# Kernel tuning notes

Measured on AMD Instinct MI355X. Metric: run time of the kernel, lower is better.

## Reference

```python
import jax, jax.numpy as jnp
import numpy as np

H, W, C = 64, 64, 2048
IMG = 224


def setup_inputs() -> dict:
    key = jax.random.key(0)
    features = jax.random.normal(key, (2, H, W, C), dtype=jnp.float32)
    return {"features": features, "img_size": IMG}


def reference(features, img_size):
    # features: [2, H, W, C] -- query (index 0) and target (index 1) feature maps.
    x0 = features[0]  # [H, W, C]
    x1 = features[1]  # [H, W, C]
    # Correlation volume: Decomposition[i,j,k,l] = sum_c x0[i,j,c] * x1[k,l,c]
    # (replaces the quadruple Python loop with a single GEMM-shaped einsum)
    decom = jnp.einsum('ijc,klc->ijkl', x0, x1)  # [H, W, H, W]
    decom = decom / jnp.max(decom)
    # NOTE: source calls `Decomposition.clamp(min=0)` without assignment -> no-op.
    decom_1 = jnp.sum(decom, axis=(2, 3))  # [H, W] saliency on query image
    decom_2 = jnp.sum(decom, axis=(0, 1))  # [H, W] saliency on target image
    stacked = jnp.stack((decom_1, decom_2))  # [2, H, W]
    # F.interpolate(mode='bilinear', align_corners=False) == half-pixel bilinear resize
    out = jax.image.resize(stacked, (2, img_size, img_size), method='bilinear')
    return out  # [2, img_size, img_size]
```

## Files before the change

### kernel.cpp

```cpp
#include <hip/hip_runtime.h>
#include <hip/hip_bf16.h>

#define HW    4096
#define CDIM  2048
#define IMG   224
#define NTKI  64
#define NTM   128
#define LROW  528
#define QSCALE 21.166666f
#define NS    32
#define SBUF  24576

typedef int   int4v  __attribute__((ext_vector_type(4)));
typedef int   i32x16 __attribute__((ext_vector_type(16)));
typedef char  char4v __attribute__((ext_vector_type(4)));

__device__ __forceinline__ i32x16 zi16() {
    i32x16 z;
#pragma unroll
    for (int i = 0; i < 16; ++i) z[i] = 0;
    return z;
}
__device__ __forceinline__ char quant8(float x) {
    int r = __float2int_rn(x * QSCALE);
    r = min(max(r, -127), 127);
    return (char)r;
}

__device__ __forceinline__ void gload_lds16(const char* g, char* l) {
    __builtin_amdgcn_global_load_lds(
        (const __attribute__((address_space(1))) void*)g,
        (__attribute__((address_space(3))) void*)l, 16, 0, 0);
}

__global__ __launch_bounds__(256) void convert_pack_partial(
    const float* __restrict__ feat,
    char* __restrict__ Ap, char* __restrict__ Bp,
    float* __restrict__ P) {
    __shared__ char lds[64 * LROW];
    __shared__ float csum[512];
    const int tid = threadIdx.x;
    const int mat = blockIdx.z;
    const int rm  = blockIdx.y;
    const int kb0 = blockIdx.x * 512;
    const float* src = feat + (size_t)mat * HW * CDIM + (size_t)(rm * 64) * CDIM + kb0;

    const int cc = (tid & 127) * 4;
    float a0 = 0.f, a1 = 0.f, a2 = 0.f, a3 = 0.f;
#pragma unroll
    for (int j = 0; j < 32; ++j) {
        const int r = j * 2 + (tid >> 7);
        float4 v = *(const float4*)&src[(size_t)r * CDIM + cc];
        a0 += v.x; a1 += v.y; a2 += v.z; a3 += v.w;
        char4v q;
        q[0] = quant8(v.x); q[1] = quant8(v.y);
        q[2] = quant8(v.z); q[3] = quant8(v.w);
        *(char4v*)&lds[r * LROW + cc] = q;
    }
    if (tid >= 128) {
        csum[cc + 0] = a0; csum[cc + 1] = a1;
        csum[cc + 2] = a2; csum[cc + 3] = a3;
    }
    __syncthreads();
    if (tid < 128) {
        float4 p;
        p.x = a0 + csum[cc + 0]; p.y = a1 + csum[cc + 1];
        p.z = a2 + csum[cc + 2]; p.w = a3 + csum[cc + 3];
        *(float4*)&P[((size_t)mat * 64 + rm) * CDIM + kb0 + cc] = p;
    }

    const int l = tid & 63, w = tid >> 6;
    char* dstbase = mat ? Bp : Ap;
#pragma unroll
    for (int i = 0; i < 8; ++i) {
        const int t = w * 8 + i;
        const int tml = t >> 4, tkl = t & 15;
        int4v v = *(const int4v*)
            &lds[(tml * 32 + (l & 31)) * LROW + tkl * 32 + (l >> 5) * 16];
        const int tm  = rm * 2 + tml;
        const int tkg = blockIdx.x * 16 + tkl;
        *(int4v*)&dstbase[((size_t)(tm * NTKI + tkg) * 64 + l) * 16] = v;
    }
}

__global__ __launch_bounds__(512, 4) void gemm_max_kernel(
    const char* __restrict__ Ap, const char* __restrict__ Bp,
    const float* __restrict__ P, float* __restrict__ s,
    float* __restrict__ blockmax) {
    __shared__ char lds[3 * SBUF];
    __shared__ int wred[8];
    const int tid  = threadIdx.x;
    const int lane = tid & 63;
    const int wave = tid >> 6;
    const int wm = wave >> 1, wn = wave & 1;
    const int bm = blockIdx.y, bn = blockIdx.x;

    const char* gb[3];
    int loff[3];
#pragma unroll
    for (int q = 0; q < 3; ++q) {
        const int c = wave * 3 + q;
        const int kk = c & 1;
        if (c < 16) {
            const int il = c >> 1;
            gb[q] = Ap + ((size_t)(bm * 8 + il) * NTKI + kk) * 1024 + lane * 16;
            loff[q] = il * 2048 + kk * 1024;
        } else {
            const int jl = (c - 16) >> 1;
            gb[q] = Bp + ((size_t)(bn * 4 + jl) * NTKI + kk) * 1024 + lane * 16;
            loff[q] = 16384 + jl * 2048 + kk * 1024;
        }
    }

#define ISSUE_STAGE(S) do {                                         \
        char* buf_ = lds + ((S) % 3) * SBUF;                        \
        _Pragma("unroll")                                           \
        for (int q = 0; q < 3; ++q)                                 \
            gload_lds16(gb[q] + (size_t)(S) * 2048, buf_ + loff[q]);\
    } while (0)

    ISSUE_STAGE(0); ISSUE_STAGE(1);

    if (bm == 15 && bn < 16 && tid < 256) {
        const int gc = bn * 256 + tid;
        const float* Pp = P + (size_t)(gc >> 11) * 64 * CDIM + (gc & 2047);
        float sum = 0.f;
#pragma unroll 8
        for (int r = 0; r < 64; ++r) sum += Pp[(size_t)r * CDIM];
        s[gc] = sum;
    }

    asm volatile("s_waitcnt vmcnt(3)" ::: "memory");
    asm volatile("s_barrier" ::: "memory");

    const int aoff = wm * 2 * 2048 + lane * 16;
    const int boff = 16384 + wn * 2 * 2048 + lane * 16;

    i32x16 acc00 = zi16(), acc01 = zi16();
    i32x16 acc10 = zi16(), acc11 = zi16();

#define MM(i, j, A, B) acc##i##j = __builtin_amdgcn_mfma_i32_32x32x32_i8(A, B, acc##i##j, 0, 0, 0)

    for (int st = 0; st < NS; ++st) {
        const char* base = lds + (st % 3) * SBUF;
        const char* ab = base + aoff;
        const char* bb = base + boff;

        int4v a0k0 = *(const int4v*)(ab);
        int4v a1k0 = *(const int4v*)(ab + 2048);
        int4v a0k1 = *(const int4v*)(ab + 1024);
        int4v a1k1 = *(const int4v*)(ab + 2048 + 1024);
        int4v b0k0 = *(const int4v*)(bb);
        int4v b1k0 = *(const int4v*)(bb + 2048);
        int4v b0k1 = *(const int4v*)(bb + 1024);
        int4v b1k1 = *(const int4v*)(bb + 2048 + 1024);

        if (st + 2 < NS) ISSUE_STAGE(st + 2);

        __builtin_amdgcn_s_setprio(1);
        MM(0,0, a0k0, b0k0); MM(0,1, a0k0, b1k0);
        MM(1,0, a1k0, b0k0); MM(1,1, a1k0, b1k0);
        MM(0,0, a0k1, b0k1); MM(0,1, a0k1, b1k1);
        MM(1,0, a1k1, b0k1); MM(1,1, a1k1, b1k1);
        __builtin_amdgcn_s_setprio(0);

        if (st < NS - 2) { asm volatile("s_waitcnt vmcnt(3)" ::: "memory"); }
        else             { asm volatile("s_waitcnt vmcnt(0)" ::: "memory"); }
        if (st < NS - 1) { asm volatile("s_barrier" ::: "memory"); }
    }
#undef ISSUE_STAGE
#undef MM

    int m = INT_MIN;
#pragma unroll
    for (int i = 0; i < 16; ++i) {
        m = max(m, acc00[i]); m = max(m, acc01[i]);
        m = max(m, acc10[i]); m = max(m, acc11[i]);
    }
#pragma unroll
    for (int off = 32; off; off >>= 1)
        m = max(m, __shfl_down(m, off));
    if (lane == 0) wred[wave] = m;
    __syncthreads();
    if (tid == 0) {
        int im = wred[0];
#pragma unroll
        for (int w2 = 1; w2 < 8; ++w2) im = max(im, wred[w2]);
        blockmax[blockIdx.y * gridDim.x + blockIdx.x] =
            (float)im * (1.0f / (QSCALE * QSCALE));
    }
}

__global__ __launch_bounds__(256) void saliency_kernel(
    const float* __restrict__ feat, const float* __restrict__ s,
    float* __restrict__ sal) {
    const int tid = threadIdx.x, lane = tid & 63, wave = tid >> 6;
    const int g = blockIdx.x * 4 + wave;
    const float* x;
    const float* sv;
    if (g < HW) { x = feat + (size_t)g * CDIM;                            sv = s + CDIM; }
    else        { x = feat + (size_t)HW * CDIM + (size_t)(g - HW) * CDIM; sv = s; }
    float acc = 0.f;
#pragma unroll
    for (int it = 0; it < 8; ++it) {
        const int c0 = it * 256 + lane * 4;
        float4 v = *(const float4*)&x[c0];
        float4 w = *(const float4*)&sv[c0];
        acc += v.x * w.x + v.y * w.y + v.z * w.z + v.w * w.w;
    }
#pragma unroll
    for (int off = 32; off; off >>= 1) acc += __shfl_down(acc, off);
    if (lane == 0) sal[g] = acc;
}

__global__ __launch_bounds__(256) void resize_kernel(
    const float* __restrict__ sal, const float* __restrict__ bmax,
    float* __restrict__ out) {
    __shared__ float w[4];
    __shared__ float rM;
    const int tid = threadIdx.x;
    float m = -3.4e38f;
    for (int i = tid; i < 512; i += 256) m = fmaxf(m, bmax[i]);
#pragma unroll
    for (int off = 32; off; off >>= 1) m = fmaxf(m, __shfl_down(m, off));
    if ((tid & 63) == 0) w[tid >> 6] = m;
    __syncthreads();
    if (tid == 0)
        rM = 1.0f / fmaxf(fmaxf(w[0], w[1]), fmaxf(w[2], w[3]));
    __syncthreads();

    const int idx = blockIdx.x * 256 + tid;
    if (idx >= 2 * IMG * IMG) return;
    const int ch = idx / (IMG * IMG);
    const int rem = idx % (IMG * IMG);
    const int oy = rem / IMG, ox = rem % IMG;
    const float scale = 64.0f / (float)IMG;
    const float sy = ((float)oy + 0.5f) * scale - 0.5f;
    const float sx = ((float)ox + 0.5f) * scale - 0.5f;
    const float fy0 = floorf(sy), fx0 = floorf(sx);
    const float wy = sy - fy0, wx = sx - fx0;
    int y0 = (int)fy0, x0 = (int)fx0;
    int y1 = min(max(y0 + 1, 0), 63), x1 = min(max(x0 + 1, 0), 63);
    y0 = min(max(y0, 0), 63); x0 = min(max(x0, 0), 63);
    const float* p = sal + ch * HW;
    const float v00 = p[y0 * 64 + x0], v01 = p[y0 * 64 + x1];
    const float v10 = p[y1 * 64 + x0], v11 = p[y1 * 64 + x1];
    out[idx] = ((1.f - wy) * ((1.f - wx) * v00 + wx * v01) +
                wy * ((1.f - wx) * v10 + wx * v11)) * rM;
}

extern "C" void kernel_launch(void* const* d_in, const int* in_sizes, int n_in,
                              void* d_out, int out_size, void* d_ws, size_t ws_size,
                              hipStream_t stream) {
    const float* feat = (const float*)d_in[0];
    float* out = (float*)d_out;

    char* ws = (char*)d_ws;
    char* Ap = ws;
    char* Bp = ws + (size_t)8 * 1024 * 1024;
    float* P    = (float*)(ws + (size_t)16 * 1024 * 1024);
    float* s    = P + 2 * 64 * CDIM;
    float* bmax = s + 2 * CDIM;
    float* sal  = bmax + 1024;

    convert_pack_partial<<<dim3(4, 64, 2), 256, 0, stream>>>(feat, Ap, Bp, P);
    gemm_max_kernel<<<dim3(32, 16), 512, 0, stream>>>(Ap, Bp, P, s, bmax);
    saliency_kernel<<<2048, 256, 0, stream>>>(feat, s, sal);
    const int nout = 2 * IMG * IMG;
    resize_kernel<<<(nout + 255) / 256, 256, 0, stream>>>(sal, bmax, out);
}
```

Baseline: 140.5 us.

## Enlarge GEMM block tile to 256x256 with 4 waves and register double-buffering

The int8 correlation GEMM now uses 256 threads per block, each wave computing a 128x128 sub-tile (4x4 MFMA accumulators) over a 16x16 grid instead of 32x16. The triple-buffered LDS stage grows to 32 KB, and LDS fragment reads for the next stage are software-pipelined against MFMAs on the current stage using two register sets. The aim is more operand reuse per LDS byte and less global traffic per output. The cost is only 256 blocks, fewer than two per CU, with one block per CU allowed, plus heavy register and accumulator pressure.

```diff
diff --git a/kernel.cpp b/kernel.cpp
--- a/kernel.cpp
+++ b/kernel.cpp
@@ -9,7 +9,7 @@
 #define LROW  528
 #define QSCALE 21.166666f
 #define NS    32
-#define SBUF  24576
+#define SBUF3 32768
 
 typedef int   int4v  __attribute__((ext_vector_type(4)));
 typedef int   i32x16 __attribute__((ext_vector_type(16)));
@@ -83,23 +83,23 @@
     }
 }
 
-__global__ __launch_bounds__(512, 4) void gemm_max_kernel(
+__global__ __launch_bounds__(256, 1) void gemm_max_kernel(
     const char* __restrict__ Ap, const char* __restrict__ Bp,
     const float* __restrict__ P, float* __restrict__ s,
     float* __restrict__ blockmax) {
-    __shared__ char lds[3 * SBUF];
-    __shared__ int wred[8];
+    __shared__ char lds[3 * SBUF3];
+    __shared__ int wred[4];
     const int tid  = threadIdx.x;
     const int lane = tid & 63;
     const int wave = tid >> 6;
     const int wm = wave >> 1, wn = wave & 1;
     const int bm = blockIdx.y, bn = blockIdx.x;
 
-    const char* gb[3];
-    int loff[3];
-#pragma unroll
-    for (int q = 0; q < 3; ++q) {
-        const int c = wave * 3 + q;
+    const char* gb[8];
+    int loff[8];
+#pragma unroll
+    for (int q = 0; q < 8; ++q) {
+        const int c = wave * 8 + q;
         const int kk = c & 1;
         if (c < 16) {
             const int il = c >> 1;
@@ -107,21 +107,24 @@
             loff[q] = il * 2048 + kk * 1024;
         } else {
             const int jl = (c - 16) >> 1;
-            gb[q] = Bp + ((size_t)(bn * 4 + jl) * NTKI + kk) * 1024 + lane * 16;
+            gb[q] = Bp + ((size_t)(bn * 8 + jl) * NTKI + kk) * 1024 + lane * 16;
             loff[q] = 16384 + jl * 2048 + kk * 1024;
         }
     }
 
-#define ISSUE_STAGE(S) do {                                         \
-        char* buf_ = lds + ((S) % 3) * SBUF;                        \
+#define ISSUE_STAGE(S, BUF) do {                                    \
         _Pragma("unroll")                                           \
-        for (int q = 0; q < 3; ++q)                                 \
-            gload_lds16(gb[q] + (size_t)(S) * 2048, buf_ + loff[q]);\
+        for (int q = 0; q < 8; ++q)                                 \
+            gload_lds16(gb[q] + (size_t)(S) * 2048, (BUF) + loff[q]);\
     } while (0)
 
-    ISSUE_STAGE(0); ISSUE_STAGE(1);
-
-    if (bm == 15 && bn < 16 && tid < 256) {
+    char* r0 = lds;
+    char* r1 = lds + SBUF3;
+    char* r2 = lds + 2 * SBUF3;
+
+    ISSUE_STAGE(0, r0); ISSUE_STAGE(1, r1);
+
+    if (bm == 15 && bn < 16) {
         const int gc = bn * 256 + tid;
         const float* Pp = P + (size_t)(gc >> 11) * 64 * CDIM + (gc & 2047);
         float sum = 0.f;
@@ -130,62 +133,96 @@
         s[gc] = sum;
     }
 
-    asm volatile("s_waitcnt vmcnt(3)" ::: "memory");
+    asm volatile("s_waitcnt vmcnt(8)" ::: "memory");
     asm volatile("s_barrier" ::: "memory");
 
-    const int aoff = wm * 2 * 2048 + lane * 16;
-    const int boff = 16384 + wn * 2 * 2048 + lane * 16;
-
-    i32x16 acc00 = zi16(), acc01 = zi16();
-    i32x16 acc10 = zi16(), acc11 = zi16();
-
-#define MM(i, j, A, B) acc##i##j = __builtin_amdgcn_mfma_i32_32x32x32_i8(A, B, acc##i##j, 0, 0, 0)
-
-    for (int st = 0; st < NS; ++st) {
-        const char* base = lds + (st % 3) * SBUF;
-        const char* ab = base + aoff;
-        const char* bb = base + boff;
-
-        int4v a0k0 = *(const int4v*)(ab);
-        int4v a1k0 = *(const int4v*)(ab + 2048);
-        int4v a0k1 = *(const int4v*)(ab + 1024);
-        int4v a1k1 = *(const int4v*)(ab + 2048 + 1024);
-        int4v b0k0 = *(const int4v*)(bb);
-        int4v b1k0 = *(const int4v*)(bb + 2048);
-        int4v b0k1 = *(const int4v*)(bb + 1024);
-        int4v b1k1 = *(const int4v*)(bb + 2048 + 1024);
-
-        if (st + 2 < NS) ISSUE_STAGE(st + 2);
-
-        __builtin_amdgcn_s_setprio(1);
-        MM(0,0, a0k0, b0k0); MM(0,1, a0k0, b1k0);
-        MM(1,0, a1k0, b0k0); MM(1,1, a1k0, b1k0);
-        MM(0,0, a0k1, b0k1); MM(0,1, a0k1, b1k1);
-        MM(1,0, a1k1, b0k1); MM(1,1, a1k1, b1k1);
-        __builtin_amdgcn_s_setprio(0);
-
-        if (st < NS - 2) { asm volatile("s_waitcnt vmcnt(3)" ::: "memory"); }
-        else             { asm volatile("s_waitcnt vmcnt(0)" ::: "memory"); }
-        if (st < NS - 1) { asm volatile("s_barrier" ::: "memory"); }
+    const int aoff = wm * 8192 + lane * 16;
+    const int boff = 16384 + wn * 8192 + lane * 16;
+
+    i32x16 acc[4][4];
+#pragma unroll
+    for (int i = 0; i < 4; ++i)
+#pragma unroll
+        for (int j = 0; j < 4; ++j) {
+            acc[i][j] = zi16();
+            asm volatile("" : "+a"(acc[i][j]));
+        }
+
+#define READ_HALF(AR, BR, BASE, KK) do {                                    \
+        _Pragma("unroll")                                                   \
+        for (int i = 0; i < 4; ++i)                                         \
+            AR[i][KK] = *(const int4v*)((BASE) + aoff + i * 2048 + (KK) * 1024); \
+        _Pragma("unroll")                                                   \
+        for (int j = 0; j < 4; ++j)                                         \
+            BR[j][KK] = *(const int4v*)((BASE) + boff + j * 2048 + (KK) * 1024); \
+    } while (0)
+
+#define MFMA_HALF(AR, BR, KK) do {                                          \
+        __builtin_amdgcn_s_setprio(1);                                      \
+        _Pragma("unroll")                                                   \
+        for (int i = 0; i < 4; ++i)                                         \
+            _Pragma("unroll")                                               \
+            for (int j = 0; j < 4; ++j)                                     \
+                acc[i][j] = __builtin_amdgcn_mfma_i32_32x32x32_i8(          \
+                    AR[i][KK], BR[j][KK], acc[i][j], 0, 0, 0);              \
+        __builtin_amdgcn_s_setprio(0);                                      \
+    } while (0)
+
+#define ROTATE() do { char* t_ = r0; r0 = r1; r1 = r2; r2 = t_; } while (0)
+
+    int4v xa[4][2], xb[4][2];
+    int4v ya[4][2], yb[4][2];
+
+    READ_HALF(xa, xb, r0, 0);
+    READ_HALF(xa, xb, r0, 1);
+
+    for (int it = 0; it < 16; ++it) {
+        if (it < 15) {
+            ISSUE_STAGE(2 * it + 2, r2);
+            asm volatile("s_waitcnt vmcnt(8)" ::: "memory");
+        } else {
+            asm volatile("s_waitcnt vmcnt(0)" ::: "memory");
+        }
+        asm volatile("s_barrier" ::: "memory");
+        READ_HALF(ya, yb, r1, 0);
+        MFMA_HALF(xa, xb, 0);
+        READ_HALF(ya, yb, r1, 1);
+        MFMA_HALF(xa, xb, 1);
+        ROTATE();
+
+        if (it < 15) {
+            ISSUE_STAGE(2 * it + 3, r2);
+            asm volatile("s_waitcnt vmcnt(8)" ::: "memory");
+        } else {
+            asm volatile("s_waitcnt vmcnt(0)" ::: "memory");
+        }
+        asm volatile("s_barrier" ::: "memory");
+        READ_HALF(xa, xb, r1, 0);
+        MFMA_HALF(ya, yb, 0);
+        READ_HALF(xa, xb, r1, 1);
+        MFMA_HALF(ya, yb, 1);
+        ROTATE();
     }
 #undef ISSUE_STAGE
-#undef MM
+#undef READ_HALF
+#undef MFMA_HALF
+#undef ROTATE
 
     int m = INT_MIN;
 #pragma unroll
-    for (int i = 0; i < 16; ++i) {
-        m = max(m, acc00[i]); m = max(m, acc01[i]);
-        m = max(m, acc10[i]); m = max(m, acc11[i]);
-    }
+    for (int i = 0; i < 4; ++i)
+#pragma unroll
+        for (int j = 0; j < 4; ++j)
+#pragma unroll
+            for (int e = 0; e < 16; ++e)
+                m = max(m, acc[i][j][e]);
 #pragma unroll
     for (int off = 32; off; off >>= 1)
         m = max(m, __shfl_down(m, off));
     if (lane == 0) wred[wave] = m;
     __syncthreads();
     if (tid == 0) {
-        int im = wred[0];
-#pragma unroll
-        for (int w2 = 1; w2 < 8; ++w2) im = max(im, wred[w2]);
+        const int im = max(max(wred[0], wred[1]), max(wred[2], wred[3]));
         blockmax[blockIdx.y * gridDim.x + blockIdx.x] =
             (float)im * (1.0f / (QSCALE * QSCALE));
     }
@@ -220,7 +257,7 @@
     __shared__ float rM;
     const int tid = threadIdx.x;
     float m = -3.4e38f;
-    for (int i = tid; i < 512; i += 256) m = fmaxf(m, bmax[i]);
+    for (int i = tid; i < 256; i += 256) m = fmaxf(m, bmax[i]);
 #pragma unroll
     for (int off = 32; off; off >>= 1) m = fmaxf(m, __shfl_down(m, off));
     if ((tid & 63) == 0) w[tid >> 6] = m;
@@ -264,7 +301,7 @@
     float* sal  = bmax + 1024;
 
     convert_pack_partial<<<dim3(4, 64, 2), 256, 0, stream>>>(feat, Ap, Bp, P);
-    gemm_max_kernel<<<dim3(32, 16), 512, 0, stream>>>(Ap, Bp, P, s, bmax);
+    gemm_max_kernel<<<dim3(16, 16), 256, 0, stream>>>(Ap, Bp, P, s, bmax);
     saliency_kernel<<<2048, 256, 0, stream>>>(feat, s, sal);
     const int nout = 2 * IMG * IMG;
     resize_kernel<<<(nout + 255) / 256, 256, 0, stream>>>(sal, bmax, out);
```

Result: no change. 140.0 us (-0.3%).
